# Optimization experiments

Hardware: AMD Instinct MI355X
Metric: run time of the kernel (lower is better)

Reference implementation:

```python
import jax, jax.numpy as jnp
import numpy as np

N_HEADS = 8
ATT_DIM = 64


def _pos_enc(x):
    # x: (chan, L, bs, D); sinusoidal PE added along axis -3 (the query/key slot dim)
    L, D = x.shape[-3], x.shape[-1]
    pos = np.arange(L)[:, None].astype(np.float32)
    div = np.exp(np.arange(0, D, 2).astype(np.float32) * (-np.log(10000.0) / D))
    pe = np.zeros((L, 1, D), dtype=np.float32)
    pe[:, 0, 0::2] = np.sin(pos * div)
    pe[:, 0, 1::2] = np.cos(pos * div)
    return x + jnp.asarray(pe)


def setup_inputs() -> dict:
    key = jax.random.key(0)
    ks = jax.random.split(key, 6)
    C, NQ, NK, B, QD, KD = 8, 16, 32, 128, 128, 128
    E = N_HEADS * ATT_DIM  # 512
    OUT = ATT_DIM  # out_dim defaults to attention_dim
    b = np.float32(1.0 / np.sqrt(ATT_DIM))
    bp = np.float32(1.0 / np.sqrt(OUT))
    return {
        "q": jax.random.normal(ks[0], (C, NQ, B, QD), dtype=jnp.float32),
        "k": jax.random.normal(ks[1], (C, NK, B, KD), dtype=jnp.float32),
        "Wq": jax.random.uniform(ks[2], (C, NQ, QD, E), jnp.float32, -b, b),
        "Wk": jax.random.uniform(ks[3], (C, NK, KD, E), jnp.float32, -b, b),
        "Wv": jax.random.uniform(ks[4], (C, NK, KD, E), jnp.float32, -b, b),
        "Wp": jax.random.uniform(ks[5], (C, NQ, E, OUT), jnp.float32, -bp, bp),
    }


def reference(q, k, Wq, Wk, Wv, Wp):
    H, A = N_HEADS, ATT_DIM
    C, NQ, B, _ = q.shape
    NK = k.shape[1]
    inv_temp = jnp.float32(1.0 / np.sqrt(A))
    q_pe = _pos_enc(q)
    k_pe = _pos_enc(k)
    # per-channel grouped QKV projections: (C, N, B, D) x (C, N, D, E) -> (C, N, B, E)
    query = jnp.einsum('cqbd,cqde->cqbe', q_pe, Wq).reshape(C, NQ, B, H, A)
    key_t = jnp.einsum('ckbd,ckde->ckbe', k_pe, Wk).reshape(C, NK, B, H, A)
    value = jnp.einsum('ckbd,ckde->ckbe', k_pe, Wv).reshape(C, NK, B, H, A)
    # attention scores per (channel, batch, head)
    logits = jnp.einsum('cqbha,ckbha->cbhqk', query, key_t) * inv_temp
    attn = jax.nn.softmax(logits, axis=-1)
    # value aggregation (original does broadcast-multiply+sum; einsum is the same math)
    out = jnp.einsum('cbhqk,ckbha->cqbha', attn, value).reshape(C, NQ, B, H * A)
    # per-channel output projection
    return jnp.einsum('cqbe,cqeo->cqbo', out, Wp)
```

## Files before the change

### kernel.cpp

```cpp
#include <hip/hip_runtime.h>

#define C_  8
#define NQ_ 16
#define NK_ 32
#define B_  128
#define D_  128
#define E_  512
#define H_  8
#define A_  64
#define O_  64

typedef __attribute__((ext_vector_type(4))) float f32x4;
typedef __attribute__((ext_vector_type(8))) short bf16x8;
typedef __attribute__((ext_vector_type(4))) short bf16x4;

__device__ __forceinline__ short f2bf(float f) {
    union { float f; unsigned u; } v; v.f = f;
    unsigned r = v.u + 0x7fffu + ((v.u >> 16) & 1u);
    return (short)(r >> 16);
}

__global__ __launch_bounds__(256) void qkv_proj_kernel(
    const float* __restrict__ qin, const float* __restrict__ kin,
    const float* __restrict__ Wq, const float* __restrict__ Wk,
    const float* __restrict__ Wv,
    short* __restrict__ wsq, short* __restrict__ wsk, short* __restrict__ wsv)
{
    __shared__ __align__(16) short Alds[B_][72];
    __shared__ __align__(16) short Blds[128][72];
    __shared__ float pe_buf[D_];

    const int tid   = threadIdx.x;
    const int blk   = blockIdx.x;
    const int e_blk = blk & 3;
    const int unit  = blk >> 2;

    const float* X; const float* W; short* Y; int n; size_t ypitch;
    if (unit < C_ * NQ_) {
        const int c = unit >> 4;
        n = unit & 15;
        X = qin + (size_t)unit * B_ * D_;
        W = Wq  + (size_t)unit * D_ * E_;
        Y = wsq + (size_t)c * B_ * NQ_ * E_ + (size_t)n * E_;
        ypitch = (size_t)NQ_ * E_;
    } else if (unit < C_ * (NQ_ + NK_)) {
        const int u = unit - C_ * NQ_;
        const int c = u >> 5;
        n = u & 31;
        X = kin + (size_t)u * B_ * D_;
        W = Wk  + (size_t)u * D_ * E_;
        Y = wsk + (size_t)c * B_ * NK_ * E_ + (size_t)n * E_;
        ypitch = (size_t)NK_ * E_;
    } else {
        const int u = unit - C_ * (NQ_ + NK_);
        const int c = u >> 5;
        n = u & 31;
        X = kin + (size_t)u * B_ * D_;
        W = Wv  + (size_t)u * D_ * E_;
        Y = wsv + (size_t)c * B_ * NK_ * E_ + (size_t)n * E_;
        ypitch = (size_t)NK_ * E_;
    }

    if (tid < D_) {
        const int d = tid;
        const float freq = expf((float)(d & ~1) * (-9.210340371976184f / (float)D_));
        const float arg  = (float)n * freq;
        pe_buf[d] = (d & 1) ? cosf(arg) : sinf(arg);
    }
    __syncthreads();

    const int wv   = tid >> 6;
    const int lane = tid & 63;
    const int lr   = lane & 15;
    const int quad = lane >> 4;
    const int wrow = (wv >> 1) * 64;
    const int wcol = (wv & 1) * 64;

    f32x4 acc[4][4];
    for (int m = 0; m < 4; ++m)
        for (int nf = 0; nf < 4; ++nf)
            acc[m][nf] = (f32x4){0.f, 0.f, 0.f, 0.f};

    const int e  = tid & 127;
    const int kg = (tid >> 7) * 32;

    for (int k0 = 0; k0 < D_; k0 += 64) {
        f32x4 a_raw[8];
        #pragma unroll
        for (int i = 0; i < 8; ++i) {
            const int id  = tid + 256 * i;
            const int row = id >> 4;
            const int ch  = id & 15;
            a_raw[i] = *(const f32x4*)(X + (size_t)row * D_ + k0 + ch * 4);
        }
        float b_raw[32];
        const float* bsrc = W + (size_t)(k0 + kg) * E_ + e_blk * 128 + e;
        #pragma unroll
        for (int i = 0; i < 32; ++i)
            b_raw[i] = bsrc[(size_t)i * E_];

        #pragma unroll
        for (int i = 0; i < 8; ++i) {
            const int id  = tid + 256 * i;
            const int row = id >> 4;
            const int ch  = id & 15;
            bf16x4 v;
            #pragma unroll
            for (int j = 0; j < 4; ++j)
                v[j] = f2bf(a_raw[i][j] + pe_buf[k0 + ch * 4 + j]);
            *(bf16x4*)&Alds[row][ch * 4] = v;
        }
        #pragma unroll
        for (int i = 0; i < 4; ++i) {
            bf16x8 v;
            #pragma unroll
            for (int j = 0; j < 8; ++j)
                v[j] = f2bf(b_raw[i * 8 + j]);
            *(bf16x8*)&Blds[e][kg + i * 8] = v;
        }
        __syncthreads();

        for (int ks = 0; ks < 2; ++ks) {
            const int kc = ks * 32 + quad * 8;
            bf16x8 af[4], bfr[4];
            for (int m = 0; m < 4; ++m)
                af[m] = *(const bf16x8*)&Alds[wrow + m * 16 + lr][kc];
            for (int nf = 0; nf < 4; ++nf)
                bfr[nf] = *(const bf16x8*)&Blds[wcol + nf * 16 + lr][kc];
            for (int m = 0; m < 4; ++m)
                for (int nf = 0; nf < 4; ++nf)
                    acc[m][nf] = __builtin_amdgcn_mfma_f32_16x16x32_bf16(
                        af[m], bfr[nf], acc[m][nf], 0, 0, 0);
        }
        __syncthreads();
    }

    for (int m = 0; m < 4; ++m)
        for (int nf = 0; nf < 4; ++nf)
            for (int r = 0; r < 4; ++r) {
                const int row = wrow + m * 16 + quad * 4 + r;
                const int col = e_blk * 128 + wcol + nf * 16 + lr;
                Y[(size_t)row * ypitch + col] = f2bf(acc[m][nf][r]);
            }
}

__global__ __launch_bounds__(256) void attn_kernel(
    const short* __restrict__ wsq, const short* __restrict__ wsk,
    const short* __restrict__ wsv, short* __restrict__ wso)
{
    __shared__ __align__(16) short Ks[32][264];
    __shared__ __align__(16) short Vs[32][258];
    __shared__ __align__(16) short Ps[4][16][40];

    const int tid = threadIdx.x;
    const int blk = blockIdx.x;
    const int hh  = blk & 1;
    const int b   = (blk >> 1) & (B_ - 1);
    const int c   = blk >> 8;

    const short* qb = wsq + ((size_t)(c * B_ + b) * NQ_) * E_ + hh * 256;
    const short* kb = wsk + ((size_t)(c * B_ + b) * NK_) * E_ + hh * 256;
    const short* vb = wsv + ((size_t)(c * B_ + b) * NK_) * E_ + hh * 256;

    const int wv   = tid >> 6;
    const int lane = tid & 63;
    const int lr   = lane & 15;
    const int quad = lane >> 4;
    const int lcol = wv * 64;

    const bf16x8 aq0 = *(const bf16x8*)(qb + (size_t)lr * E_ + lcol + quad * 8);
    const bf16x8 aq1 = *(const bf16x8*)(qb + (size_t)lr * E_ + lcol + 32 + quad * 8);

    {
        const int nloc = tid >> 5;
        const int ch   = tid & 31;
        #pragma unroll
        for (int i = 0; i < 4; ++i) {
            const int nn = nloc + i * 8;
            *(bf16x8*)&Ks[nn][ch * 8] = *(const bf16x8*)(kb + (size_t)nn * E_ + ch * 8);
        }
        #pragma unroll
        for (int i = 0; i < 4; ++i) {
            const int nn = nloc + i * 8;
            bf16x8 v = *(const bf16x8*)(vb + (size_t)nn * E_ + ch * 8);
            #pragma unroll
            for (int p = 0; p < 4; ++p)
                *(int*)&Vs[nn][ch * 8 + p * 2] = ((const int*)&v)[p];
        }
    }
    __syncthreads();

    f32x4 sacc0 = (f32x4){0.f, 0.f, 0.f, 0.f};
    f32x4 sacc1 = (f32x4){0.f, 0.f, 0.f, 0.f};
    #pragma unroll
    for (int ks = 0; ks < 2; ++ks) {
        const int kc = lcol + ks * 32 + quad * 8;
        const bf16x8 aq  = ks ? aq1 : aq0;
        const bf16x8 bk0 = *(const bf16x8*)&Ks[lr][kc];
        const bf16x8 bk1 = *(const bf16x8*)&Ks[16 + lr][kc];
        sacc0 = __builtin_amdgcn_mfma_f32_16x16x32_bf16(aq, bk0, sacc0, 0, 0, 0);
        sacc1 = __builtin_amdgcn_mfma_f32_16x16x32_bf16(aq, bk1, sacc1, 0, 0, 0);
    }

    float p0[4], p1[4];
    for (int r = 0; r < 4; ++r) {
        const float v0 = sacc0[r] * 0.125f;
        const float v1 = sacc1[r] * 0.125f;
        float m = fmaxf(v0, v1);
        m = fmaxf(m, __shfl_xor(m, 1));
        m = fmaxf(m, __shfl_xor(m, 2));
        m = fmaxf(m, __shfl_xor(m, 4));
        m = fmaxf(m, __shfl_xor(m, 8));
        const float e0 = __expf(v0 - m);
        const float e1 = __expf(v1 - m);
        float s = e0 + e1;
        s += __shfl_xor(s, 1);
        s += __shfl_xor(s, 2);
        s += __shfl_xor(s, 4);
        s += __shfl_xor(s, 8);
        const float inv = 1.0f / s;
        p0[r] = e0 * inv;
        p1[r] = e1 * inv;
    }

    for (int r = 0; r < 4; ++r) {
        Ps[wv][quad * 4 + r][lr]      = f2bf(p0[r]);
        Ps[wv][quad * 4 + r][16 + lr] = f2bf(p1[r]);
    }
    __syncthreads();
    const bf16x8 ap = *(const bf16x8*)&Ps[wv][lr][quad * 8];

    #pragma unroll
    for (int t = 0; t < 4; ++t) {
        bf16x8 bvv;
        #pragma unroll
        for (int j = 0; j < 8; ++j)
            bvv[j] = Vs[quad * 8 + j][lcol + t * 16 + lr];
        f32x4 oacc = (f32x4){0.f, 0.f, 0.f, 0.f};
        oacc = __builtin_amdgcn_mfma_f32_16x16x32_bf16(ap, bvv, oacc, 0, 0, 0);
        for (int r = 0; r < 4; ++r)
            wso[((size_t)(c * NQ_ + quad * 4 + r) * B_ + b) * E_
                + hh * 256 + lcol + t * 16 + lr] = f2bf(oacc[r]);
    }
}

__global__ __launch_bounds__(256) void out_proj_kernel(
    const short* __restrict__ wso, const float* __restrict__ Wp,
    float* __restrict__ out)
{
    __shared__ __align__(16) short Xlds[32][72];
    __shared__ __align__(16) short Wlds[32][72];

    const int tid = threadIdx.x;
    const int blk = blockIdx.x;
    const int cq  = blk >> 3;
    const int bh  = (blk >> 1) & 3;
    const int oh  = blk & 1;

    const short* Xb = wso + (size_t)cq * B_ * E_ + (size_t)bh * 32 * E_;
    const float* Wb = Wp  + (size_t)cq * E_ * O_ + oh * 32;
    float*       Ob = out + (size_t)cq * B_ * O_ + (size_t)bh * 32 * O_ + oh * 32;

    const int wv   = tid >> 6;
    const int lane = tid & 63;
    const int lr   = lane & 15;
    const int quad = lane >> 4;
    const int rowh = wv >> 1;
    const int ohh  = wv & 1;
    const int o    = tid & 31;
    const int kg   = tid >> 5;

    f32x4 acc = (f32x4){0.f, 0.f, 0.f, 0.f};

    bf16x8 xv[2];
    float  wr[2][8];

    auto issue = [&](int s, int buf) {
        const int k0 = s * 64;
        xv[buf] = *(const bf16x8*)(Xb + (size_t)(tid >> 3) * E_ + k0 + (tid & 7) * 8);
        #pragma unroll
        for (int j = 0; j < 8; ++j)
            wr[buf][j] = Wb[(size_t)(k0 + kg * 8 + j) * O_ + o];
    };

    issue(0, 0);
    #pragma unroll
    for (int s = 0; s < 8; ++s) {
        const int cb = s & 1;
        if (s < 7) issue(s + 1, cb ^ 1);

        *(bf16x8*)&Xlds[tid >> 3][(tid & 7) * 8] = xv[cb];
        bf16x8 wv8;
        #pragma unroll
        for (int j = 0; j < 8; ++j) wv8[j] = f2bf(wr[cb][j]);
        *(bf16x8*)&Wlds[o][kg * 8] = wv8;
        __syncthreads();

        #pragma unroll
        for (int ks = 0; ks < 2; ++ks) {
            const int kc = ks * 32 + quad * 8;
            const bf16x8 af  = *(const bf16x8*)&Xlds[rowh * 16 + lr][kc];
            const bf16x8 bfr = *(const bf16x8*)&Wlds[ohh * 16 + lr][kc];
            acc = __builtin_amdgcn_mfma_f32_16x16x32_bf16(af, bfr, acc, 0, 0, 0);
        }
        __syncthreads();
    }

    #pragma unroll
    for (int r = 0; r < 4; ++r)
        Ob[(size_t)(rowh * 16 + quad * 4 + r) * O_ + ohh * 16 + lr] = acc[r];
}

extern "C" void kernel_launch(void* const* d_in, const int* in_sizes, int n_in,
                              void* d_out, int out_size, void* d_ws, size_t ws_size,
                              hipStream_t stream) {
    const float* q  = (const float*)d_in[0];
    const float* k  = (const float*)d_in[1];
    const float* Wq = (const float*)d_in[2];
    const float* Wk = (const float*)d_in[3];
    const float* Wv = (const float*)d_in[4];
    const float* Wp = (const float*)d_in[5];
    float* out = (float*)d_out;

    const size_t sz_q = (size_t)C_ * NQ_ * B_ * E_;
    const size_t sz_k = (size_t)C_ * NK_ * B_ * E_;
    short* wsq = (short*)d_ws;
    short* wsk = wsq + sz_q;
    short* wsv = wsk + sz_k;
    short* wso = wsv + sz_k;

    qkv_proj_kernel<<<dim3(2560), dim3(256), 0, stream>>>(q, k, Wq, Wk, Wv, wsq, wsk, wsv);
    attn_kernel<<<dim3(2048), dim3(256), 0, stream>>>(wsq, wsk, wsv, wso);
    out_proj_kernel<<<dim3(1024), dim3(256), 0, stream>>>(wso, Wp, out);
}
```

Before: 250.0 us.

## Process both head halves per attention block with prefetch; preload whole K in out_proj

```diff
diff --git a/kernel.cpp b/kernel.cpp
--- a/kernel.cpp
+++ b/kernel.cpp
@@ -153,103 +153,132 @@
     __shared__ __align__(16) short Ps[4][16][40];
 
     const int tid = threadIdx.x;
-    const int blk = blockIdx.x;
-    const int hh  = blk & 1;
-    const int b   = (blk >> 1) & (B_ - 1);
-    const int c   = blk >> 8;
-
-    const short* qb = wsq + ((size_t)(c * B_ + b) * NQ_) * E_ + hh * 256;
-    const short* kb = wsk + ((size_t)(c * B_ + b) * NK_) * E_ + hh * 256;
-    const short* vb = wsv + ((size_t)(c * B_ + b) * NK_) * E_ + hh * 256;
+    const int pb  = blockIdx.x;
+    const int b   = pb & (B_ - 1);
+    const int c   = pb >> 7;
+
+    const short* qb0 = wsq + ((size_t)(c * B_ + b) * NQ_) * E_;
+    const short* kb0 = wsk + ((size_t)(c * B_ + b) * NK_) * E_;
+    const short* vb0 = wsv + ((size_t)(c * B_ + b) * NK_) * E_;
+    short*       ob0 = wso + ((size_t)(c * NQ_) * B_ + b) * E_;
 
     const int wv   = tid >> 6;
     const int lane = tid & 63;
     const int lr   = lane & 15;
     const int quad = lane >> 4;
     const int lcol = wv * 64;
-
-    const bf16x8 aq0 = *(const bf16x8*)(qb + (size_t)lr * E_ + lcol + quad * 8);
-    const bf16x8 aq1 = *(const bf16x8*)(qb + (size_t)lr * E_ + lcol + 32 + quad * 8);
-
-    {
-        const int nloc = tid >> 5;
-        const int ch   = tid & 31;
-        #pragma unroll
-        for (int i = 0; i < 4; ++i) {
-            const int nn = nloc + i * 8;
-            *(bf16x8*)&Ks[nn][ch * 8] = *(const bf16x8*)(kb + (size_t)nn * E_ + ch * 8);
-        }
-        #pragma unroll
-        for (int i = 0; i < 4; ++i) {
-            const int nn = nloc + i * 8;
-            bf16x8 v = *(const bf16x8*)(vb + (size_t)nn * E_ + ch * 8);
+    const int nloc = tid >> 5;
+    const int ch   = tid & 31;
+
+    auto loadKV = [&](const short* kb, const short* vb,
+                      bf16x8 (&kr)[4], bf16x8 (&vr)[4]) {
+        #pragma unroll
+        for (int i = 0; i < 4; ++i)
+            kr[i] = *(const bf16x8*)(kb + (size_t)(nloc + i * 8) * E_ + ch * 8);
+        #pragma unroll
+        for (int i = 0; i < 4; ++i)
+            vr[i] = *(const bf16x8*)(vb + (size_t)(nloc + i * 8) * E_ + ch * 8);
+    };
+    auto writeKV = [&](bf16x8 (&kr)[4], bf16x8 (&vr)[4]) {
+        #pragma unroll
+        for (int i = 0; i < 4; ++i)
+            *(bf16x8*)&Ks[nloc + i * 8][ch * 8] = kr[i];
+        #pragma unroll
+        for (int i = 0; i < 4; ++i)
             #pragma unroll
             for (int p = 0; p < 4; ++p)
-                *(int*)&Vs[nn][ch * 8 + p * 2] = ((const int*)&v)[p];
-        }
-    }
-    __syncthreads();
-
-    f32x4 sacc0 = (f32x4){0.f, 0.f, 0.f, 0.f};
-    f32x4 sacc1 = (f32x4){0.f, 0.f, 0.f, 0.f};
-    #pragma unroll
-    for (int ks = 0; ks < 2; ++ks) {
-        const int kc = lcol + ks * 32 + quad * 8;
-        const bf16x8 aq  = ks ? aq1 : aq0;
-        const bf16x8 bk0 = *(const bf16x8*)&Ks[lr][kc];
-        const bf16x8 bk1 = *(const bf16x8*)&Ks[16 + lr][kc];
-        sacc0 = __builtin_amdgcn_mfma_f32_16x16x32_bf16(aq, bk0, sacc0, 0, 0, 0);
-        sacc1 = __builtin_amdgcn_mfma_f32_16x16x32_bf16(aq, bk1, sacc1, 0, 0, 0);
-    }
-
-    float p0[4], p1[4];
-    for (int r = 0; r < 4; ++r) {
-        const float v0 = sacc0[r] * 0.125f;
-        const float v1 = sacc1[r] * 0.125f;
-        float m = fmaxf(v0, v1);
-        m = fmaxf(m, __shfl_xor(m, 1));
-        m = fmaxf(m, __shfl_xor(m, 2));
-        m = fmaxf(m, __shfl_xor(m, 4));
-        m = fmaxf(m, __shfl_xor(m, 8));
-        const float e0 = __expf(v0 - m);
-        const float e1 = __expf(v1 - m);
-        float s = e0 + e1;
-        s += __shfl_xor(s, 1);
-        s += __shfl_xor(s, 2);
-        s += __shfl_xor(s, 4);
-        s += __shfl_xor(s, 8);
-        const float inv = 1.0f / s;
-        p0[r] = e0 * inv;
-        p1[r] = e1 * inv;
-    }
-
-    for (int r = 0; r < 4; ++r) {
-        Ps[wv][quad * 4 + r][lr]      = f2bf(p0[r]);
-        Ps[wv][quad * 4 + r][16 + lr] = f2bf(p1[r]);
-    }
-    __syncthreads();
-    const bf16x8 ap = *(const bf16x8*)&Ps[wv][lr][quad * 8];
-
-    #pragma unroll
-    for (int t = 0; t < 4; ++t) {
-        bf16x8 bvv;
-        #pragma unroll
-        for (int j = 0; j < 8; ++j)
-            bvv[j] = Vs[quad * 8 + j][lcol + t * 16 + lr];
-        f32x4 oacc = (f32x4){0.f, 0.f, 0.f, 0.f};
-        oacc = __builtin_amdgcn_mfma_f32_16x16x32_bf16(ap, bvv, oacc, 0, 0, 0);
-        for (int r = 0; r < 4; ++r)
-            wso[((size_t)(c * NQ_ + quad * 4 + r) * B_ + b) * E_
-                + hh * 256 + lcol + t * 16 + lr] = f2bf(oacc[r]);
-    }
+                *(int*)&Vs[nloc + i * 8][ch * 8 + p * 2] = ((const int*)&vr[i])[p];
+    };
+
+    auto computeUnit = [&](const short* qb, short* ob) {
+        const bf16x8 aq0 = *(const bf16x8*)(qb + (size_t)lr * E_ + lcol + quad * 8);
+        const bf16x8 aq1 = *(const bf16x8*)(qb + (size_t)lr * E_ + lcol + 32 + quad * 8);
+
+        f32x4 sacc0 = (f32x4){0.f, 0.f, 0.f, 0.f};
+        f32x4 sacc1 = (f32x4){0.f, 0.f, 0.f, 0.f};
+        {
+            const int kc0 = lcol + quad * 8;
+            sacc0 = __builtin_amdgcn_mfma_f32_16x16x32_bf16(aq0, *(const bf16x8*)&Ks[lr][kc0], sacc0, 0, 0, 0);
+            sacc1 = __builtin_amdgcn_mfma_f32_16x16x32_bf16(aq0, *(const bf16x8*)&Ks[16 + lr][kc0], sacc1, 0, 0, 0);
+            const int kc1 = lcol + 32 + quad * 8;
+            sacc0 = __builtin_amdgcn_mfma_f32_16x16x32_bf16(aq1, *(const bf16x8*)&Ks[lr][kc1], sacc0, 0, 0, 0);
+            sacc1 = __builtin_amdgcn_mfma_f32_16x16x32_bf16(aq1, *(const bf16x8*)&Ks[16 + lr][kc1], sacc1, 0, 0, 0);
+        }
+
+        float p0[4], p1[4];
+        #pragma unroll
+        for (int r = 0; r < 4; ++r) {
+            const float v0 = sacc0[r] * 0.125f;
+            const float v1 = sacc1[r] * 0.125f;
+            float m = fmaxf(v0, v1);
+            m = fmaxf(m, __shfl_xor(m, 1));
+            m = fmaxf(m, __shfl_xor(m, 2));
+            m = fmaxf(m, __shfl_xor(m, 4));
+            m = fmaxf(m, __shfl_xor(m, 8));
+            const float e0 = __expf(v0 - m);
+            const float e1 = __expf(v1 - m);
+            float s = e0 + e1;
+            s += __shfl_xor(s, 1);
+            s += __shfl_xor(s, 2);
+            s += __shfl_xor(s, 4);
+            s += __shfl_xor(s, 8);
+            const float inv = 1.0f / s;
+            p0[r] = e0 * inv;
+            p1[r] = e1 * inv;
+        }
+
+        #pragma unroll
+        for (int r = 0; r < 4; ++r) {
+            Ps[wv][quad * 4 + r][lr]      = f2bf(p0[r]);
+            Ps[wv][quad * 4 + r][16 + lr] = f2bf(p1[r]);
+        }
+        __syncthreads();
+        const bf16x8 ap = *(const bf16x8*)&Ps[wv][lr][quad * 8];
+
+        short* Osb = ((short*)Ks) + wv * 1024;
+
+        #pragma unroll
+        for (int t = 0; t < 4; ++t) {
+            bf16x8 bvv;
+            #pragma unroll
+            for (int j = 0; j < 8; ++j)
+                bvv[j] = Vs[quad * 8 + j][lcol + t * 16 + lr];
+            f32x4 oacc = (f32x4){0.f, 0.f, 0.f, 0.f};
+            oacc = __builtin_amdgcn_mfma_f32_16x16x32_bf16(ap, bvv, oacc, 0, 0, 0);
+            #pragma unroll
+            for (int r = 0; r < 4; ++r)
+                Osb[(quad * 4 + r) * 64 + t * 16 + lr] = f2bf(oacc[r]);
+        }
+
+        const int q   = lane >> 2;
+        const int seg = lane & 3;
+        const bf16x8 oA = *(const bf16x8*)&Osb[q * 64 + seg * 16];
+        const bf16x8 oB = *(const bf16x8*)&Osb[q * 64 + seg * 16 + 8];
+        short* dst = ob + (size_t)q * (B_ * E_) + lcol + seg * 16;
+        *(bf16x8*)dst       = oA;
+        *(bf16x8*)(dst + 8) = oB;
+    };
+
+    bf16x8 kr0[4], vr0[4], kr1[4], vr1[4];
+    loadKV(kb0, vb0, kr0, vr0);
+    writeKV(kr0, vr0);
+    __syncthreads();
+
+    loadKV(kb0 + 256, vb0 + 256, kr1, vr1);
+    computeUnit(qb0, ob0);
+    __syncthreads();
+
+    writeKV(kr1, vr1);
+    __syncthreads();
+    computeUnit(qb0 + 256, ob0 + 256);
 }
 
 __global__ __launch_bounds__(256) void out_proj_kernel(
     const short* __restrict__ wso, const float* __restrict__ Wp,
     float* __restrict__ out)
 {
-    __shared__ __align__(16) short Xlds[32][72];
-    __shared__ __align__(16) short Wlds[32][72];
+    __shared__ __align__(16) short Xlds[32 * 512];
+    __shared__ __align__(16) short Wlds[32 * 512];
 
     const int tid = threadIdx.x;
     const int blk = blockIdx.x;
@@ -260,6 +289,38 @@
     const short* Xb = wso + (size_t)cq * B_ * E_ + (size_t)bh * 32 * E_;
     const float* Wb = Wp  + (size_t)cq * E_ * O_ + oh * 32;
     float*       Ob = out + (size_t)cq * B_ * O_ + (size_t)bh * 32 * O_ + oh * 32;
+
+    const int xrow = tid >> 3;
+    const int xch  = tid & 7;
+    const int o    = tid & 31;
+    const int kg   = tid >> 5;
+
+    bf16x8 xv[8];
+    #pragma unroll
+    for (int s = 0; s < 8; ++s)
+        xv[s] = *(const bf16x8*)(Xb + (size_t)xrow * E_ + s * 64 + xch * 8);
+
+    float wr[8][8];
+    #pragma unroll
+    for (int s = 0; s < 8; ++s)
+        #pragma unroll
+        for (int j = 0; j < 8; ++j)
+            wr[s][j] = Wb[(size_t)(s * 64 + kg * 8 + j) * O_ + o];
+
+    #pragma unroll
+    for (int s = 0; s < 8; ++s) {
+        const int g = (s * 8 + xch) ^ (xrow & 7);
+        *(bf16x8*)&Xlds[xrow * 512 + g * 8] = xv[s];
+    }
+    #pragma unroll
+    for (int s = 0; s < 8; ++s) {
+        bf16x8 w8;
+        #pragma unroll
+        for (int j = 0; j < 8; ++j) w8[j] = f2bf(wr[s][j]);
+        const int g = (s * 8 + kg) ^ (o & 7);
+        *(bf16x8*)&Wlds[o * 512 + g * 8] = w8;
+    }
+    __syncthreads();
 
     const int wv   = tid >> 6;
     const int lane = tid & 63;
@@ -267,43 +328,17 @@
     const int quad = lane >> 4;
     const int rowh = wv >> 1;
     const int ohh  = wv & 1;
-    const int o    = tid & 31;
-    const int kg   = tid >> 5;
+    const int arow = rowh * 16 + lr;
+    const int brow = ohh * 16 + lr;
 
     f32x4 acc = (f32x4){0.f, 0.f, 0.f, 0.f};
-
-    bf16x8 xv[2];
-    float  wr[2][8];
-
-    auto issue = [&](int s, int buf) {
-        const int k0 = s * 64;
-        xv[buf] = *(const bf16x8*)(Xb + (size_t)(tid >> 3) * E_ + k0 + (tid & 7) * 8);
-        #pragma unroll
-        for (int j = 0; j < 8; ++j)
-            wr[buf][j] = Wb[(size_t)(k0 + kg * 8 + j) * O_ + o];
-    };
-
-    issue(0, 0);
-    #pragma unroll
-    for (int s = 0; s < 8; ++s) {
-        const int cb = s & 1;
-        if (s < 7) issue(s + 1, cb ^ 1);
-
-        *(bf16x8*)&Xlds[tid >> 3][(tid & 7) * 8] = xv[cb];
-        bf16x8 wv8;
-        #pragma unroll
-        for (int j = 0; j < 8; ++j) wv8[j] = f2bf(wr[cb][j]);
-        *(bf16x8*)&Wlds[o][kg * 8] = wv8;
-        __syncthreads();
-
-        #pragma unroll
-        for (int ks = 0; ks < 2; ++ks) {
-            const int kc = ks * 32 + quad * 8;
-            const bf16x8 af  = *(const bf16x8*)&Xlds[rowh * 16 + lr][kc];
-            const bf16x8 bfr = *(const bf16x8*)&Wlds[ohh * 16 + lr][kc];
-            acc = __builtin_amdgcn_mfma_f32_16x16x32_bf16(af, bfr, acc, 0, 0, 0);
-        }
-        __syncthreads();
+    #pragma unroll
+    for (int st = 0; st < 16; ++st) {
+        const int ga = (st * 4 + quad) ^ (arow & 7);
+        const int gb = (st * 4 + quad) ^ (brow & 7);
+        const bf16x8 af  = *(const bf16x8*)&Xlds[arow * 512 + ga * 8];
+        const bf16x8 bfr = *(const bf16x8*)&Wlds[brow * 512 + gb * 8];
+        acc = __builtin_amdgcn_mfma_f32_16x16x32_bf16(af, bfr, acc, 0, 0, 0);
     }
 
     #pragma unroll
@@ -330,6 +365,6 @@
     short* wso = wsv + sz_k;
 
     qkv_proj_kernel<<<dim3(2560), dim3(256), 0, stream>>>(q, k, Wq, Wk, Wv, wsq, wsk, wsv);
-    attn_kernel<<<dim3(2048), dim3(256), 0, stream>>>(wsq, wsk, wsv, wso);
+    attn_kernel<<<dim3(1024), dim3(256), 0, stream>>>(wsq, wsk, wsv, wso);
     out_proj_kernel<<<dim3(1024), dim3(256), 0, stream>>>(wso, Wp, out);
 }
```

New measurement: 252.4 us. No clear change (+1.0%).
